# Performance work log

Measured on AMD Instinct MI355X. Metric: run time of the kernel, lower is better.

Reference implementation:

```python
import jax, jax.numpy as jnp
import numpy as np

NB_HEAD = 16
SIZE_PER_HEAD = 64
D_MODEL = 1024
OUT_DIM = NB_HEAD * SIZE_PER_HEAD
BIG_NEG = 1e10


def setup_inputs() -> dict:
    key = jax.random.key(0)
    ks = jax.random.split(key, 6)
    B, L = 2, 2048
    q = jax.random.normal(ks[0], (B, L, D_MODEL), dtype=jnp.float32)
    k = jax.random.normal(ks[1], (B, L, D_MODEL), dtype=jnp.float32)
    v = jax.random.normal(ks[2], (B, L, D_MODEL), dtype=jnp.float32)
    v_mask = jnp.ones((B, L), dtype=jnp.float32)
    q_mask = jnp.ones((B, L), dtype=jnp.float32)
    # glorot_normal-ish init for the three projection kernels
    std = (2.0 / (D_MODEL + OUT_DIM)) ** 0.5
    q_kernel = jax.random.normal(ks[3], (D_MODEL, OUT_DIM), dtype=jnp.float32) * std
    k_kernel = jax.random.normal(ks[4], (D_MODEL, OUT_DIM), dtype=jnp.float32) * std
    v_kernel = jax.random.normal(ks[5], (D_MODEL, OUT_DIM), dtype=jnp.float32) * std
    return {"q": q, "k": k, "v": v, "v_mask": v_mask, "q_mask": q_mask,
            "q_kernel": q_kernel, "k_kernel": k_kernel, "v_kernel": v_kernel}


def reference(q, k, v, v_mask, q_mask, q_kernel, k_kernel, v_kernel):
    B, Lq, _ = q.shape
    Lk = k.shape[1]
    H, D = NB_HEAD, SIZE_PER_HEAD
    # projections -> [B, L, H, D]
    qw = (q @ q_kernel).reshape(B, Lq, H, D)
    kw = (k @ k_kernel).reshape(B, Lk, H, D)
    vw = (v @ v_kernel).reshape(B, Lk, H, D)
    # scaled dot-product scores [B, H, Lq, Lk]
    scores = jnp.einsum('bqhd,bkhd->bhqk', qw, kw) / jnp.sqrt(jnp.float32(D))
    # additive key mask (original permutes so mask broadcasts over key axis)
    scores = scores - (1.0 - v_mask)[:, None, None, :] * BIG_NEG
    a = jax.nn.softmax(scores, axis=-1)
    # weighted sum -> [B, Lq, H, D] -> [B, Lq, H*D]
    o = jnp.einsum('bhqk,bkhd->bqhd', a, vw).reshape(B, Lq, H * D)
    # multiplicative query mask on output
    o = o * q_mask[:, :, None]
    return o
```

## Files before the change

kernel.cpp:

```cpp
#include <hip/hip_runtime.h>
#include <hip/hip_bf16.h>

#define B_SZ 2
#define SEQ  2048
#define DM   1024
#define NH   16
#define HD   64

typedef __attribute__((ext_vector_type(8))) short bf16x8;
typedef __attribute__((ext_vector_type(4))) short bf16x4;
typedef __attribute__((ext_vector_type(4))) float f32x4;
typedef __attribute__((ext_vector_type(16))) float f32x16;

__device__ __forceinline__ short f2b(float f) {
    __hip_bfloat16 h = __float2bfloat16(f);
    return *reinterpret_cast<short*>(&h);
}

__device__ __forceinline__ void async_copy16(void* lds, const void* g) {
    __builtin_amdgcn_global_load_lds(
        (const __attribute__((address_space(1))) void*)g,
        (__attribute__((address_space(3))) void*)lds, 16, 0, 0);
}

__global__ __launch_bounds__(256) void kPre(
    const float* __restrict__ q, const float* __restrict__ k, const float* __restrict__ v,
    const float* __restrict__ w0, const float* __restrict__ w1, const float* __restrict__ w2,
    short* __restrict__ qb, short* __restrict__ kb, short* __restrict__ vb,
    short* __restrict__ t0, short* __restrict__ t1, short* __restrict__ t2) {
    int z = blockIdx.z, tid = threadIdx.x;
    if (z < 3) {
        const float* src = z == 0 ? q : (z == 1 ? k : v);
        short*       dst = z == 0 ? qb : (z == 1 ? kb : vb);
        size_t i = ((size_t)blockIdx.x * 256 + tid) * 8;
        float4 a0 = *reinterpret_cast<const float4*>(src + i);
        float4 a1 = *reinterpret_cast<const float4*>(src + i + 4);
        bf16x8 c;
        c[0] = f2b(a0.x); c[1] = f2b(a0.y); c[2] = f2b(a0.z); c[3] = f2b(a0.w);
        c[4] = f2b(a1.x); c[5] = f2b(a1.y); c[6] = f2b(a1.z); c[7] = f2b(a1.w);
        *reinterpret_cast<bf16x8*>(dst + i) = c;
    } else {
        if (blockIdx.x >= 256) return;
        const float* w = z == 3 ? w0 : (z == 4 ? w1 : w2);
        short*       t = z == 3 ? t0 : (z == 4 ? t1 : t2);
        __shared__ float tile[64][65];
        int n0 = (blockIdx.x & 15) * 64, k0 = (blockIdx.x >> 4) * 64;
        int c = tid & 63, rr = tid >> 6;
#pragma unroll
        for (int i = 0; i < 16; i++) {
            int kk = i * 4 + rr;
            tile[kk][c] = w[(size_t)(k0 + kk) * DM + n0 + c];
        }
        __syncthreads();
#pragma unroll
        for (int i = 0; i < 16; i++) {
            int nn = i * 4 + rr;
            t[(size_t)(n0 + nn) * DM + k0 + c] = f2b(tile[c][nn]);
        }
    }
}

__global__ __launch_bounds__(256) void kProj(
    const short* __restrict__ qb, const short* __restrict__ kb, const short* __restrict__ vb,
    const short* __restrict__ wtq, const short* __restrict__ wtk, const short* __restrict__ wtv,
    short* __restrict__ qw, short* __restrict__ kw, short* __restrict__ vwT) {
    int z = blockIdx.z;
    const short* A  = z == 0 ? qb : (z == 1 ? kb : vb);
    const short* Bt = z == 0 ? wtq : (z == 1 ? wtk : wtv);

    __shared__ short As[128 * 64];
    __shared__ short Bs[128 * 64];

    int tid = threadIdx.x;
    int m0 = blockIdx.y * 128, n0 = blockIdx.x * 128;
    int wv = tid >> 6, lane = tid & 63, quad = lane >> 4, ln = lane & 15;
    int rblk = (wv >> 1) * 64, cblk = (wv & 1) * 64;

    int rA = wv * 32;
    int srow = rA + (lane >> 3), scol = (lane & 7) * 8;

    f32x4 zero = {0.f, 0.f, 0.f, 0.f};
    f32x4 acc[4][4];
#pragma unroll
    for (int rt = 0; rt < 4; rt++)
#pragma unroll
        for (int ct = 0; ct < 4; ct++) acc[rt][ct] = zero;

    for (int ks = 0; ks < DM; ks += 64) {
        const short* gA = A  + (size_t)(m0 + srow) * DM + ks + scol;
        const short* gB = Bt + (size_t)(n0 + srow) * DM + ks + scol;
#pragma unroll
        for (int i = 0; i < 4; i++) {
            async_copy16(&As[(rA + i * 8) * 64], gA + (size_t)i * 8 * DM);
            async_copy16(&Bs[(rA + i * 8) * 64], gB + (size_t)i * 8 * DM);
        }
        __syncthreads();
#pragma unroll
        for (int kc = 0; kc < 2; kc++) {
            bf16x8 af[4], bfv[4];
#pragma unroll
            for (int rt = 0; rt < 4; rt++)
                af[rt] = *reinterpret_cast<bf16x8*>(&As[(rblk + rt * 16 + ln) * 64 + kc * 32 + quad * 8]);
#pragma unroll
            for (int ct = 0; ct < 4; ct++)
                bfv[ct] = *reinterpret_cast<bf16x8*>(&Bs[(cblk + ct * 16 + ln) * 64 + kc * 32 + quad * 8]);
#pragma unroll
            for (int rt = 0; rt < 4; rt++)
#pragma unroll
                for (int ct = 0; ct < 4; ct++)
                    acc[rt][ct] = __builtin_amdgcn_mfma_f32_16x16x32_bf16(
                        af[rt], bfv[ct], acc[rt][ct], 0, 0, 0);
        }
        __syncthreads();
    }

    if (z < 2) {
        short* C = z == 0 ? qw : kw;
#pragma unroll
        for (int rt = 0; rt < 4; rt++)
#pragma unroll
            for (int r = 0; r < 4; r++) {
                int row = m0 + rblk + rt * 16 + quad * 4 + r;
#pragma unroll
                for (int ct = 0; ct < 4; ct++)
                    C[(size_t)row * DM + n0 + cblk + ct * 16 + ln] = f2b(acc[rt][ct][r]);
            }
    } else {
#pragma unroll
        for (int rt = 0; rt < 4; rt++) {
            int srow0 = m0 + rblk + rt * 16 + quad * 4;
            int bb = srow0 >> 11, lk = srow0 & (SEQ - 1);
#pragma unroll
            for (int ct = 0; ct < 4; ct++) {
                int coln = n0 + cblk + ct * 16 + ln;
                int hh = coln >> 6, dd = coln & 63;
                bf16x4 pk;
                pk[0] = f2b(acc[rt][ct][0]); pk[1] = f2b(acc[rt][ct][1]);
                pk[2] = f2b(acc[rt][ct][2]); pk[3] = f2b(acc[rt][ct][3]);
                *reinterpret_cast<bf16x4*>(
                    &vwT[(((size_t)bb * NH + hh) * HD + dd) * SEQ + lk]) = pk;
            }
        }
    }
}

__global__ __launch_bounds__(256, 2) void kAttn(
    const short* __restrict__ qw, const short* __restrict__ kw, const short* __restrict__ vwT,
    const float* __restrict__ vmask, const float* __restrict__ qmask, float* __restrict__ out) {
    int b = blockIdx.z, h = blockIdx.y, lq0 = blockIdx.x * 128;
    int tid = threadIdx.x, wv = tid >> 6, lane = tid & 63;
    int l5 = lane & 31, half = lane >> 5;

    __shared__ short Ks[128][72];
    __shared__ short Vt[64][136];
    __shared__ short Ps[4][32][136];

    const short* qrow = qw + (size_t)(b * SEQ + lq0 + wv * 32 + l5) * DM + h * HD;
    bf16x8 qf[4];
#pragma unroll
    for (int ki = 0; ki < 4; ki++)
        qf[ki] = *reinterpret_cast<const bf16x8*>(qrow + ki * 16 + half * 8);

    float lrow = 0.f;
    f32x16 o0, o1;
#pragma unroll
    for (int i = 0; i < 16; i++) { o0[i] = 0.f; o1[i] = 0.f; }

    int krow = tid >> 1, kcol = (tid & 1) * 32;
    int vrow = tid >> 2, vcol = (tid & 3) * 32;
    const short* kp = kw + (size_t)(b * SEQ + krow) * DM + h * HD + kcol;
    const short* vp = vwT + ((size_t)(b * NH + h) * HD + vrow) * SEQ + vcol;
    const float* vmb = vmask + b * SEQ;

    bf16x8 kr[4], vr[4];
#pragma unroll
    for (int i = 0; i < 4; i++) {
        kr[i] = *reinterpret_cast<const bf16x8*>(kp + i * 8);
        vr[i] = *reinterpret_cast<const bf16x8*>(vp + i * 8);
    }

    for (int it = 0; it < SEQ / 128; it++) {
        int lk0 = it * 128;
#pragma unroll
        for (int i = 0; i < 4; i++) {
            *reinterpret_cast<bf16x8*>(&Ks[krow][kcol + i * 8]) = kr[i];
            *reinterpret_cast<bf16x8*>(&Vt[vrow][vcol + i * 8]) = vr[i];
        }
        __syncthreads();

        if (it + 1 < SEQ / 128) {
            kp += (size_t)128 * DM;
            vp += 128;
#pragma unroll
            for (int i = 0; i < 4; i++) {
                kr[i] = *reinterpret_cast<const bf16x8*>(kp + i * 8);
                vr[i] = *reinterpret_cast<const bf16x8*>(vp + i * 8);
            }
        }

        f32x16 s[4];
#pragma unroll
        for (int lt = 0; lt < 4; lt++)
#pragma unroll
            for (int i = 0; i < 16; i++) s[lt][i] = 0.f;
#pragma unroll
        for (int lt = 0; lt < 4; lt++)
#pragma unroll
            for (int ki = 0; ki < 4; ki++) {
                bf16x8 kf = *reinterpret_cast<bf16x8*>(&Ks[lt * 32 + l5][ki * 16 + half * 8]);
                s[lt] = __builtin_amdgcn_mfma_f32_32x32x16_bf16(kf, qf[ki], s[lt], 0, 0, 0);
            }

        float rs = 0.f;
#pragma unroll
        for (int lt = 0; lt < 4; lt++)
#pragma unroll
            for (int g = 0; g < 4; g++) {
                float4 mv = *reinterpret_cast<const float4*>(
                    &vmb[lk0 + lt * 32 + 8 * g + 4 * half]);
                float p0 = __expf(s[lt][4 * g + 0] * 0.125f - (1.0f - mv.x) * 1e10f);
                float p1 = __expf(s[lt][4 * g + 1] * 0.125f - (1.0f - mv.y) * 1e10f);
                float p2 = __expf(s[lt][4 * g + 2] * 0.125f - (1.0f - mv.z) * 1e10f);
                float p3 = __expf(s[lt][4 * g + 3] * 0.125f - (1.0f - mv.w) * 1e10f);
                rs += (p0 + p1) + (p2 + p3);
                bf16x4 pk;
                pk[0] = f2b(p0); pk[1] = f2b(p1); pk[2] = f2b(p2); pk[3] = f2b(p3);
                *reinterpret_cast<bf16x4*>(&Ps[wv][l5][lt * 32 + 8 * g + 4 * half]) = pk;
            }
        rs += __shfl_xor(rs, 32);
        lrow += rs;

        bf16x8 pf[8];
#pragma unroll
        for (int ki = 0; ki < 8; ki++)
            pf[ki] = *reinterpret_cast<bf16x8*>(&Ps[wv][l5][ki * 16 + half * 8]);

#pragma unroll
        for (int ki = 0; ki < 8; ki++) {
            bf16x8 vf0 = *reinterpret_cast<bf16x8*>(&Vt[l5][ki * 16 + half * 8]);
            bf16x8 vf1 = *reinterpret_cast<bf16x8*>(&Vt[32 + l5][ki * 16 + half * 8]);
            o0 = __builtin_amdgcn_mfma_f32_32x32x16_bf16(vf0, pf[ki], o0, 0, 0, 0);
            o1 = __builtin_amdgcn_mfma_f32_32x32x16_bf16(vf1, pf[ki], o1, 0, 0, 0);
        }
        __syncthreads();
    }

    int lq = lq0 + wv * 32 + l5;
    float sc2 = (1.0f / lrow) * qmask[b * SEQ + lq];
    float* orow = out + (size_t)(b * SEQ + lq) * DM + h * HD;
#pragma unroll
    for (int g = 0; g < 4; g++) {
        float4 st0, st1;
        st0.x = o0[4 * g + 0] * sc2; st0.y = o0[4 * g + 1] * sc2;
        st0.z = o0[4 * g + 2] * sc2; st0.w = o0[4 * g + 3] * sc2;
        st1.x = o1[4 * g + 0] * sc2; st1.y = o1[4 * g + 1] * sc2;
        st1.z = o1[4 * g + 2] * sc2; st1.w = o1[4 * g + 3] * sc2;
        *reinterpret_cast<float4*>(&orow[8 * g + 4 * half]) = st0;
        *reinterpret_cast<float4*>(&orow[32 + 8 * g + 4 * half]) = st1;
    }
}

extern "C" void kernel_launch(void* const* d_in, const int* in_sizes, int n_in,
                              void* d_out, int out_size, void* d_ws, size_t ws_size,
                              hipStream_t stream) {
    const float* q  = (const float*)d_in[0];
    const float* k  = (const float*)d_in[1];
    const float* v  = (const float*)d_in[2];
    const float* vm = (const float*)d_in[3];
    const float* qm = (const float*)d_in[4];
    const float* qk = (const float*)d_in[5];
    const float* kk = (const float*)d_in[6];
    const float* vk = (const float*)d_in[7];
    float* out = (float*)d_out;

    short* ws  = (short*)d_ws;
    short* wtq = ws;
    short* wtk = wtq + 1024 * 1024;
    short* wtv = wtk + 1024 * 1024;
    short* vb  = wtv + 1024 * 1024;
    short* qw  = vb + (size_t)4096 * 1024;
    short* kw  = qw + (size_t)4096 * 1024;
    short* vwT = kw + (size_t)4096 * 1024;
    short* qb = (short*)d_out;
    short* kb = qb + (size_t)4096 * 1024;

    kPre <<<dim3(2048, 1, 6), 256, 0, stream>>>(q, k, v, qk, kk, vk,
                                                qb, kb, vb, wtq, wtk, wtv);
    kProj<<<dim3(8, 32, 3), 256, 0, stream>>>(qb, kb, vb, wtq, wtk, wtv, qw, kw, vwT);
    kAttn<<<dim3(16, 16, 2), 256, 0, stream>>>(qw, kw, vwT, vm, qm, out);
}
```

Before: 233.9 us.

## Fuse fp32-to-bf16 input conversion into projection GEMM and keep P in registers

Drops the separate activation conversion pass. The projection GEMM now loads fp32 q/k/v directly, converts them to bf16 and stores them into a padded LDS tile, which removes a full round trip of the inputs through global memory. In attention, the probability tile no longer goes through LDS: the packed bf16 values are exchanged between wave halves with shuffles to build the MFMA B operand, and exp is rewritten as exp2 with a fused multiply-add. The trade-off is that A loads become synchronous VGPR loads instead of async global-to-LDS copies, so each projection block reads fp32 A tiles (twice the bytes) repeatedly across the 8 column blocks.

```diff
diff --git a/kernel.cpp b/kernel.cpp
--- a/kernel.cpp
+++ b/kernel.cpp
@@ -11,10 +11,16 @@
 typedef __attribute__((ext_vector_type(4))) short bf16x4;
 typedef __attribute__((ext_vector_type(4))) float f32x4;
 typedef __attribute__((ext_vector_type(16))) float f32x16;
+typedef unsigned long long ull;
 
 __device__ __forceinline__ short f2b(float f) {
     __hip_bfloat16 h = __float2bfloat16(f);
     return *reinterpret_cast<short*>(&h);
+}
+__device__ __forceinline__ ull pack4(float a, float b, float c, float d) {
+    union { bf16x4 v; ull u; } t;
+    t.v[0] = f2b(a); t.v[1] = f2b(b); t.v[2] = f2b(c); t.v[3] = f2b(d);
+    return t.u;
 }
 
 __device__ __forceinline__ void async_copy16(void* lds, const void* g) {
@@ -23,52 +29,37 @@
         (__attribute__((address_space(3))) void*)lds, 16, 0, 0);
 }
 
-__global__ __launch_bounds__(256) void kPre(
+__global__ __launch_bounds__(256) void kT(
+    const float* __restrict__ w0, const float* __restrict__ w1, const float* __restrict__ w2,
+    short* __restrict__ t0, short* __restrict__ t1, short* __restrict__ t2) {
+    const float* w = blockIdx.z == 0 ? w0 : (blockIdx.z == 1 ? w1 : w2);
+    short*       t = blockIdx.z == 0 ? t0 : (blockIdx.z == 1 ? t1 : t2);
+    __shared__ float tile[64][65];
+    int n0 = (blockIdx.x & 15) * 64, k0 = (blockIdx.x >> 4) * 64;
+    int tid = threadIdx.x;
+    int c = tid & 63, rr = tid >> 6;
+#pragma unroll
+    for (int i = 0; i < 16; i++) {
+        int kk = i * 4 + rr;
+        tile[kk][c] = w[(size_t)(k0 + kk) * DM + n0 + c];
+    }
+    __syncthreads();
+#pragma unroll
+    for (int i = 0; i < 16; i++) {
+        int nn = i * 4 + rr;
+        t[(size_t)(n0 + nn) * DM + k0 + c] = f2b(tile[c][nn]);
+    }
+}
+
+__global__ __launch_bounds__(256) void kProj(
     const float* __restrict__ q, const float* __restrict__ k, const float* __restrict__ v,
-    const float* __restrict__ w0, const float* __restrict__ w1, const float* __restrict__ w2,
-    short* __restrict__ qb, short* __restrict__ kb, short* __restrict__ vb,
-    short* __restrict__ t0, short* __restrict__ t1, short* __restrict__ t2) {
-    int z = blockIdx.z, tid = threadIdx.x;
-    if (z < 3) {
-        const float* src = z == 0 ? q : (z == 1 ? k : v);
-        short*       dst = z == 0 ? qb : (z == 1 ? kb : vb);
-        size_t i = ((size_t)blockIdx.x * 256 + tid) * 8;
-        float4 a0 = *reinterpret_cast<const float4*>(src + i);
-        float4 a1 = *reinterpret_cast<const float4*>(src + i + 4);
-        bf16x8 c;
-        c[0] = f2b(a0.x); c[1] = f2b(a0.y); c[2] = f2b(a0.z); c[3] = f2b(a0.w);
-        c[4] = f2b(a1.x); c[5] = f2b(a1.y); c[6] = f2b(a1.z); c[7] = f2b(a1.w);
-        *reinterpret_cast<bf16x8*>(dst + i) = c;
-    } else {
-        if (blockIdx.x >= 256) return;
-        const float* w = z == 3 ? w0 : (z == 4 ? w1 : w2);
-        short*       t = z == 3 ? t0 : (z == 4 ? t1 : t2);
-        __shared__ float tile[64][65];
-        int n0 = (blockIdx.x & 15) * 64, k0 = (blockIdx.x >> 4) * 64;
-        int c = tid & 63, rr = tid >> 6;
-#pragma unroll
-        for (int i = 0; i < 16; i++) {
-            int kk = i * 4 + rr;
-            tile[kk][c] = w[(size_t)(k0 + kk) * DM + n0 + c];
-        }
-        __syncthreads();
-#pragma unroll
-        for (int i = 0; i < 16; i++) {
-            int nn = i * 4 + rr;
-            t[(size_t)(n0 + nn) * DM + k0 + c] = f2b(tile[c][nn]);
-        }
-    }
-}
-
-__global__ __launch_bounds__(256) void kProj(
-    const short* __restrict__ qb, const short* __restrict__ kb, const short* __restrict__ vb,
     const short* __restrict__ wtq, const short* __restrict__ wtk, const short* __restrict__ wtv,
     short* __restrict__ qw, short* __restrict__ kw, short* __restrict__ vwT) {
     int z = blockIdx.z;
-    const short* A  = z == 0 ? qb : (z == 1 ? kb : vb);
+    const float* A  = z == 0 ? q : (z == 1 ? k : v);
     const short* Bt = z == 0 ? wtq : (z == 1 ? wtk : wtv);
 
-    __shared__ short As[128 * 64];
+    __shared__ short As[128 * 72];
     __shared__ short Bs[128 * 64];
 
     int tid = threadIdx.x;
@@ -76,8 +67,9 @@
     int wv = tid >> 6, lane = tid & 63, quad = lane >> 4, ln = lane & 15;
     int rblk = (wv >> 1) * 64, cblk = (wv & 1) * 64;
 
-    int rA = wv * 32;
-    int srow = rA + (lane >> 3), scol = (lane & 7) * 8;
+    int rB = wv * 32;
+    int srowB = rB + (lane >> 3), scolB = (lane & 7) * 8;
+    int sr = tid >> 4, sc4 = (tid & 15) * 4;
 
     f32x4 zero = {0.f, 0.f, 0.f, 0.f};
     f32x4 acc[4][4];
@@ -87,12 +79,17 @@
         for (int ct = 0; ct < 4; ct++) acc[rt][ct] = zero;
 
     for (int ks = 0; ks < DM; ks += 64) {
-        const short* gA = A  + (size_t)(m0 + srow) * DM + ks + scol;
-        const short* gB = Bt + (size_t)(n0 + srow) * DM + ks + scol;
-#pragma unroll
-        for (int i = 0; i < 4; i++) {
-            async_copy16(&As[(rA + i * 8) * 64], gA + (size_t)i * 8 * DM);
-            async_copy16(&Bs[(rA + i * 8) * 64], gB + (size_t)i * 8 * DM);
+        const short* gB = Bt + (size_t)(n0 + srowB) * DM + ks + scolB;
+#pragma unroll
+        for (int i = 0; i < 4; i++)
+            async_copy16(&Bs[(rB + i * 8) * 64], gB + (size_t)i * 8 * DM);
+#pragma unroll
+        for (int i = 0; i < 8; i++) {
+            int row = i * 16 + sr;
+            float4 av = *reinterpret_cast<const float4*>(
+                &A[(size_t)(m0 + row) * DM + ks + sc4]);
+            *reinterpret_cast<ull*>(&As[row * 72 + sc4]) =
+                pack4(av.x, av.y, av.z, av.w);
         }
         __syncthreads();
 #pragma unroll
@@ -100,7 +97,7 @@
             bf16x8 af[4], bfv[4];
 #pragma unroll
             for (int rt = 0; rt < 4; rt++)
-                af[rt] = *reinterpret_cast<bf16x8*>(&As[(rblk + rt * 16 + ln) * 64 + kc * 32 + quad * 8]);
+                af[rt] = *reinterpret_cast<bf16x8*>(&As[(rblk + rt * 16 + ln) * 72 + kc * 32 + quad * 8]);
 #pragma unroll
             for (int ct = 0; ct < 4; ct++)
                 bfv[ct] = *reinterpret_cast<bf16x8*>(&Bs[(cblk + ct * 16 + ln) * 64 + kc * 32 + quad * 8]);
@@ -134,11 +131,9 @@
             for (int ct = 0; ct < 4; ct++) {
                 int coln = n0 + cblk + ct * 16 + ln;
                 int hh = coln >> 6, dd = coln & 63;
-                bf16x4 pk;
-                pk[0] = f2b(acc[rt][ct][0]); pk[1] = f2b(acc[rt][ct][1]);
-                pk[2] = f2b(acc[rt][ct][2]); pk[3] = f2b(acc[rt][ct][3]);
-                *reinterpret_cast<bf16x4*>(
-                    &vwT[(((size_t)bb * NH + hh) * HD + dd) * SEQ + lk]) = pk;
+                *reinterpret_cast<ull*>(
+                    &vwT[(((size_t)bb * NH + hh) * HD + dd) * SEQ + lk]) =
+                    pack4(acc[rt][ct][0], acc[rt][ct][1], acc[rt][ct][2], acc[rt][ct][3]);
             }
         }
     }
@@ -153,7 +148,9 @@
 
     __shared__ short Ks[128][72];
     __shared__ short Vt[64][136];
-    __shared__ short Ps[4][32][136];
+
+    const float C1 = 0.18033688f;
+    const float MB = 1.4426950e10f;
 
     const short* qrow = qw + (size_t)(b * SEQ + lq0 + wv * 32 + l5) * DM + h * HD;
     bf16x8 qf[4];
@@ -212,35 +209,36 @@
             }
 
         float rs = 0.f;
+        ull pk[4][4];
 #pragma unroll
         for (int lt = 0; lt < 4; lt++)
 #pragma unroll
             for (int g = 0; g < 4; g++) {
                 float4 mv = *reinterpret_cast<const float4*>(
                     &vmb[lk0 + lt * 32 + 8 * g + 4 * half]);
-                float p0 = __expf(s[lt][4 * g + 0] * 0.125f - (1.0f - mv.x) * 1e10f);
-                float p1 = __expf(s[lt][4 * g + 1] * 0.125f - (1.0f - mv.y) * 1e10f);
-                float p2 = __expf(s[lt][4 * g + 2] * 0.125f - (1.0f - mv.z) * 1e10f);
-                float p3 = __expf(s[lt][4 * g + 3] * 0.125f - (1.0f - mv.w) * 1e10f);
+                float p0 = exp2f(fmaf(s[lt][4 * g + 0], C1, (mv.x - 1.0f) * MB));
+                float p1 = exp2f(fmaf(s[lt][4 * g + 1], C1, (mv.y - 1.0f) * MB));
+                float p2 = exp2f(fmaf(s[lt][4 * g + 2], C1, (mv.z - 1.0f) * MB));
+                float p3 = exp2f(fmaf(s[lt][4 * g + 3], C1, (mv.w - 1.0f) * MB));
                 rs += (p0 + p1) + (p2 + p3);
-                bf16x4 pk;
-                pk[0] = f2b(p0); pk[1] = f2b(p1); pk[2] = f2b(p2); pk[3] = f2b(p3);
-                *reinterpret_cast<bf16x4*>(&Ps[wv][l5][lt * 32 + 8 * g + 4 * half]) = pk;
+                pk[lt][g] = pack4(p0, p1, p2, p3);
             }
         rs += __shfl_xor(rs, 32);
         lrow += rs;
 
-        bf16x8 pf[8];
-#pragma unroll
-        for (int ki = 0; ki < 8; ki++)
-            pf[ki] = *reinterpret_cast<bf16x8*>(&Ps[wv][l5][ki * 16 + half * 8]);
-
 #pragma unroll
         for (int ki = 0; ki < 8; ki++) {
+            int lt = ki >> 1, mb = 2 * (ki & 1);
+            ull mine = half ? pk[lt][mb + 1] : pk[lt][mb];
+            ull send = half ? pk[lt][mb]     : pk[lt][mb + 1];
+            ull rec  = __shfl_xor((long long)send, 32);
+            union { ull u[2]; bf16x8 v; } fr;
+            fr.u[0] = half ? rec : mine;
+            fr.u[1] = half ? mine : rec;
             bf16x8 vf0 = *reinterpret_cast<bf16x8*>(&Vt[l5][ki * 16 + half * 8]);
             bf16x8 vf1 = *reinterpret_cast<bf16x8*>(&Vt[32 + l5][ki * 16 + half * 8]);
-            o0 = __builtin_amdgcn_mfma_f32_32x32x16_bf16(vf0, pf[ki], o0, 0, 0, 0);
-            o1 = __builtin_amdgcn_mfma_f32_32x32x16_bf16(vf1, pf[ki], o1, 0, 0, 0);
+            o0 = __builtin_amdgcn_mfma_f32_32x32x16_bf16(vf0, fr.v, o0, 0, 0, 0);
+            o1 = __builtin_amdgcn_mfma_f32_32x32x16_bf16(vf1, fr.v, o1, 0, 0, 0);
         }
         __syncthreads();
     }
@@ -277,15 +275,11 @@
     short* wtq = ws;
     short* wtk = wtq + 1024 * 1024;
     short* wtv = wtk + 1024 * 1024;
-    short* vb  = wtv + 1024 * 1024;
-    short* qw  = vb + (size_t)4096 * 1024;
+    short* qw  = wtv + 1024 * 1024;
     short* kw  = qw + (size_t)4096 * 1024;
     short* vwT = kw + (size_t)4096 * 1024;
-    short* qb = (short*)d_out;
-    short* kb = qb + (size_t)4096 * 1024;
-
-    kPre <<<dim3(2048, 1, 6), 256, 0, stream>>>(q, k, v, qk, kk, vk,
-                                                qb, kb, vb, wtq, wtk, wtv);
-    kProj<<<dim3(8, 32, 3), 256, 0, stream>>>(qb, kb, vb, wtq, wtk, wtv, qw, kw, vwT);
+
+    kT   <<<dim3(256, 1, 3), 256, 0, stream>>>(qk, kk, vk, wtq, wtk, wtv);
+    kProj<<<dim3(8, 32, 3), 256, 0, stream>>>(q, k, v, wtq, wtk, wtv, qw, kw, vwT);
     kAttn<<<dim3(16, 16, 2), 256, 0, stream>>>(qw, kw, vwT, vm, qm, out);
 }
```

Result: slower. 240.6 us (+2.9%).
